# Performance work log

Hardware: AMD Instinct MI355X
Metric: run time of the kernel (lower is better)

## Reference

```python
import jax, jax.numpy as jnp
import numpy as np
from jax.scipy.linalg import expm

D = 12   # Fock cutoff dimension
M = 4    # qumodes per circuit
L = 2    # CVNN layers
K = M * (M - 1) // 2  # beamsplitters per interferometer
B = 1024

def _lad():
    # annihilation operator a in truncated Fock basis
    return jnp.diag(jnp.sqrt(jnp.arange(1, D, dtype=jnp.float32)), k=1).astype(jnp.complex64)

def _disp_gen(rr, ph):
    # generator of Displacement(r, phi): alpha*adag - conj(alpha)*a
    lad = _lad()
    alpha = (rr * jnp.exp(1j * ph)).astype(jnp.complex64)
    return alpha * lad.conj().T - jnp.conj(alpha) * lad

def _squeeze_mat(rr, ph):
    lad = _lad()
    z = (rr * jnp.exp(1j * ph)).astype(jnp.complex64)
    a2 = lad @ lad
    return expm(0.5 * (jnp.conj(z) * a2 - z * a2.conj().T))

def _rot_diag(ph):
    n = jnp.arange(D, dtype=jnp.float32)
    return jnp.exp(1j * ph * n).astype(jnp.complex64)

def _kerr_diag(kap):
    n = jnp.arange(D, dtype=jnp.float32)
    return jnp.exp(1j * kap * n * n).astype(jnp.complex64)

def _bs_mat(th, ph):
    # Beamsplitter exp(theta*(e^{i phi} a b^dag - e^{-i phi} a^dag b)) on D^2 space
    lad = _lad()
    eye = jnp.eye(D, dtype=jnp.complex64)
    a1 = jnp.kron(lad, eye)
    a2 = jnp.kron(eye, lad)
    H = th * (jnp.exp(1j * ph) * (a1 @ a2.conj().T) - jnp.exp(-1j * ph) * (a1.conj().T @ a2))
    return expm(H.astype(jnp.complex64)).reshape(D, D, D, D)

def _apply_1mode(psi, U, mode):
    psi = jnp.moveaxis(psi, mode + 1, -1)
    psi = psi @ U.T
    return jnp.moveaxis(psi, -1, mode + 1)

def _apply_1mode_batched(psi, U, mode):
    psi = jnp.moveaxis(psi, mode + 1, -1)
    psi = jnp.einsum('bij,b...j->b...i', U, psi)
    return jnp.moveaxis(psi, -1, mode + 1)

def _apply_diag(psi, d, mode):
    shape = [1] * psi.ndim
    shape[mode + 1] = D
    return psi * d.reshape(shape)

def _apply_2mode(psi, G, mode):
    psi = jnp.moveaxis(psi, (mode + 1, mode + 2), (-2, -1))
    psi = jnp.einsum('ijkl,...kl->...ij', G, psi)
    return jnp.moveaxis(psi, (-2, -1), (mode + 1, mode + 2))

def _interferometer(psi, theta, phi, varphi):
    # PennyLane rectangular (Clements) mesh, then per-mode rotations
    n = 0
    for ll in range(M):
        for kk in range(M - 1):
            if (ll + kk) % 2 != 1:
                psi = _apply_2mode(psi, _bs_mat(theta[n], phi[n]), kk)
                n += 1
    for m in range(M):
        psi = _apply_diag(psi, _rot_diag(varphi[m]), m)
    return psi

def _forward(x, theta_1, phi_1, varphi_1, r, phi_r, theta_2, phi_2, varphi_2, a, phi_a, k):
    b = x.shape[0]
    psi = jnp.zeros((b,) + (D,) * M, dtype=jnp.complex64)
    psi = psi.at[(slice(None),) + (0,) * M].set(1.0)  # vacuum
    # Amplitude_Phase encoding: Displacement(x[:, m], x[:, m+M]) on mode m
    for m in range(M):
        U = jax.vmap(lambda rr, ph: expm(_disp_gen(rr, ph)))(x[:, m], x[:, m + M])
        psi = _apply_1mode_batched(psi, U, m)
    # CVNeuralNetLayers
    for l in range(L):
        psi = _interferometer(psi, theta_1[l], phi_1[l], varphi_1[l])
        for m in range(M):
            psi = _apply_1mode(psi, _squeeze_mat(r[l, m], phi_r[l, m]), m)
        psi = _interferometer(psi, theta_2[l], phi_2[l], varphi_2[l])
        for m in range(M):
            psi = _apply_1mode(psi, expm(_disp_gen(a[l, m], phi_a[l, m])), m)
            psi = _apply_diag(psi, _kerr_diag(k[l, m]), m)
    # X-quadrature expvals (SF convention hbar=2: X = a + adag)
    lad = _lad()
    Xmat = lad + lad.conj().T
    sum_axes = tuple(range(1, M + 1))
    outs = [jnp.real(jnp.sum(jnp.conj(psi) * _apply_1mode(psi, Xmat, m), axis=sum_axes)) for m in range(M)]
    return jnp.stack(outs, axis=1)

def setup_inputs():
    key = jax.random.key(0)
    ks = jax.random.split(key, 12)
    tp = 2.0 * np.pi
    return {
        'x': jax.random.normal(ks[0], (B, 2 * M), dtype=jnp.float32),
        'theta_1': tp * jax.random.uniform(ks[1], (L, K), dtype=jnp.float32),
        'phi_1': tp * jax.random.uniform(ks[2], (L, K), dtype=jnp.float32),
        'varphi_1': tp * jax.random.uniform(ks[3], (L, M), dtype=jnp.float32),
        'r': 0.1 * jax.random.uniform(ks[4], (L, M), dtype=jnp.float32),
        'phi_r': tp * jax.random.uniform(ks[5], (L, M), dtype=jnp.float32),
        'theta_2': tp * jax.random.uniform(ks[6], (L, K), dtype=jnp.float32),
        'phi_2': tp * jax.random.uniform(ks[7], (L, K), dtype=jnp.float32),
        'varphi_2': tp * jax.random.uniform(ks[8], (L, M), dtype=jnp.float32),
        'a': 0.1 * jax.random.uniform(ks[9], (L, M), dtype=jnp.float32),
        'phi_a': tp * jax.random.uniform(ks[10], (L, M), dtype=jnp.float32),
        'k': tp * jax.random.uniform(ks[11], (L, M), dtype=jnp.float32),
    }

def reference(x, theta_1, phi_1, varphi_1, r, phi_r, theta_2, phi_2, varphi_2, a, phi_a, k):
    return _forward(x, theta_1, phi_1, varphi_1, r, phi_r, theta_2, phi_2, varphi_2, a, phi_a, k)
```

## Files before the change

### kernel.cpp

```cpp
#include <hip/hip_runtime.h>
#include <math.h>

#define D4 20736
#define ST 14
#define SST 168
#define KP 18

typedef float c32 __attribute__((ext_vector_type(2)));

__device__ __forceinline__ c32 C2(float x, float y) { c32 r; r.x = x; r.y = y; return r; }
#define CZERO C2(0.f, 0.f)

__device__ __forceinline__ c32 cmul(c32 a, c32 b) {
  return C2(a.x * b.x - a.y * b.y, a.x * b.y + a.y * b.x);
}
__device__ __forceinline__ c32 cfma_s(c32 a, c32 b, c32 acc) {
  acc.x = fmaf(a.x, b.x, fmaf(-a.y, b.y, acc.x));
  acc.y = fmaf(a.x, b.y, fmaf(a.y, b.x, acc.y));
  return acc;
}
__device__ __forceinline__ c32 cfma(c32 g, c32 v, c32 acc) {
  c32 t, d;
  asm("v_pk_fma_f32 %0, %1, %2, %3 op_sel_hi:[0,1,1]"
      : "=v"(t) : "v"(g), "v"(v), "v"(acc));
  asm("v_pk_fma_f32 %0, %1, %2, %3 op_sel:[1,1,0] op_sel_hi:[1,0,1] neg_lo:[1,0,0]"
      : "=v"(d) : "v"(g), "v"(v), "v"(t));
  return d;
}
__device__ __forceinline__ c32 get2(const float4* w, int n) {
  float4 q = w[n >> 1];
  return (n & 1) ? C2(q.z, q.w) : C2(q.x, q.y);
}
__device__ __forceinline__ float4 pack2(c32 a, c32 b) {
  return make_float4(a.x, a.y, b.x, b.y);
}

__constant__ int d_secoff[24] = {0,1,5,14,30,55,91,140,204,285,385,506,650,
                                 771,871,952,1016,1065,1101,1126,1142,1151,1155,1156};

__constant__ unsigned char d_perm[144] = {
  11,22,33,44,55,66,77,88,99,110,121,132,
  10,21,32,43,54,65,76,87,98,109,120,
  23,34,45,56,67,78,89,100,111,122,133,
  9,20,31,42,53,64,75,86,97,108,
  35,46,57,68,79,90,101,112,123,134,
  8,19,30,41,52,63,74,85,96,
  47,58,69,80,91,102,113,124,135,
  7,18,29,40,51,62,73,84,
  59,70,81,92,103,114,125,136,
  6,17,28,39,50,61,72,
  71,82,93,104,115,126,137,
  5,16,27,38,49,60,
  83,94,105,116,127,138,
  4,15,26,37,48,
  95,106,117,128,139,
  3,14,25,36,
  107,118,129,140,
  2,13,24,
  119,130,141,
  1,12,
  131,142,
  0,
  143
};

struct RM { int goff, sz, a0, da, r0, dr; };
__device__ __forceinline__ RM rmeta(int r) {
  const int i = r / 12, j = r - 12 * i, N = i + j;
  const bool up = (N <= 11);
  RM m;
  m.sz = (up ? N : 22 - N) + 1;
  const int lo = up ? 0 : (N - 11);
  m.goff = d_secoff[N] + (i - lo);
  m.a0 = up ? N : (143 + N);
  m.da = up ? 13 : -13;
  m.r0 = up ? N : (121 + N);
  m.dr = up ? 11 : -11;
  return m;
}

__device__ void small_expm(c32* A, c32* S, c32* P, c32* T, float* red, int sz, int tid) {
  const int n2 = sz * sz;
  if (tid < sz) {
    float s = 0.f;
    for (int j = 0; j < sz; ++j) { c32 v = A[tid * sz + j]; s += sqrtf(fmaf(v.x, v.x, v.y * v.y)); }
    red[tid] = s;
  }
  __syncthreads();
  float nrm = 0.f;
  for (int i = 0; i < sz; ++i) nrm = fmaxf(nrm, red[i]);
  int sp = 0;
  while (nrm > 0.35f && sp < 24) { nrm *= 0.5f; ++sp; }
  const float scale = ldexpf(1.f, -sp);
  for (int e = tid; e < n2; e += 64) { A[e].x *= scale; A[e].y *= scale; }
  __syncthreads();
  for (int e = tid; e < n2; e += 64) {
    c32 a = A[e];
    P[e] = a;
    if ((e / sz) == (e % sz)) a.x += 1.f;
    S[e] = a;
  }
  __syncthreads();
  for (int k = 2; k <= 12; ++k) {
    const float inv = 1.f / (float)k;
    for (int e = tid; e < n2; e += 64) {
      int i = e / sz, j = e - i * sz;
      c32 acc = CZERO;
      for (int q = 0; q < sz; ++q) acc = cfma_s(P[i * sz + q], A[q * sz + j], acc);
      acc.x *= inv; acc.y *= inv;
      T[e] = acc;
    }
    __syncthreads();
    for (int e = tid; e < n2; e += 64) {
      c32 t = T[e];
      P[e] = t;
      S[e].x += t.x; S[e].y += t.y;
    }
    __syncthreads();
  }
  for (int q = 0; q < sp; ++q) {
    for (int e = tid; e < n2; e += 64) {
      int i = e / sz, j = e - i * sz;
      c32 acc = CZERO;
      for (int w = 0; w < sz; ++w) acc = cfma_s(S[i * sz + w], S[w * sz + j], acc);
      T[e] = acc;
    }
    __syncthreads();
    for (int e = tid; e < n2; e += 64) S[e] = T[e];
    __syncthreads();
  }
}

__global__ __launch_bounds__(64) void prep_disp(const float* __restrict__ x, c32* __restrict__ c0) {
  __shared__ c32 A[144], S[144], P[144], T[144];
  __shared__ float red[12];
  const int tid = threadIdx.x;
  const int b = blockIdx.x >> 2, m = blockIdx.x & 3;
  const float rr = x[b * 8 + m], ph = x[b * 8 + 4 + m];
  float sn, cs;
  sincosf(ph, &sn, &cs);
  const c32 alpha = C2(rr * cs, rr * sn);
  for (int e = tid; e < 144; e += 64) A[e] = CZERO;
  __syncthreads();
  if (tid < 11) {
    float sq = sqrtf((float)(tid + 1));
    A[(tid + 1) * 12 + tid] = C2(alpha.x * sq, alpha.y * sq);
    A[tid * 12 + tid + 1] = C2(-alpha.x * sq, alpha.y * sq);
  }
  __syncthreads();
  small_expm(A, S, P, T, red, 12, tid);
  if (tid < 12) c0[(size_t)blockIdx.x * 12 + tid] = S[tid * 12];
}

__global__ __launch_bounds__(64) void prep_bs(const float* __restrict__ th1, const float* __restrict__ ph1,
                                              const float* __restrict__ th2, const float* __restrict__ ph2,
                                              c32* __restrict__ BS) {
  __shared__ c32 A[144], S[144], P[144], T[144];
  __shared__ float red[12];
  const int tid = threadIdx.x;
  const int g = blockIdx.x / 23, N = blockIdx.x % 23;
  const int l = g / 12, rem = g % 12, w = rem / 6, gi = rem % 6;
  const float th = (w ? th2 : th1)[l * 6 + gi];
  const float ph = (w ? ph2 : ph1)[l * 6 + gi];
  const int lo = (N > 11) ? (N - 11) : 0;
  const int sz = (N <= 11) ? (N + 1) : (23 - N);
  float sn, cs;
  sincosf(ph, &sn, &cs);
  for (int e = tid; e < sz * sz; e += 64) A[e] = CZERO;
  __syncthreads();
  if (tid + 1 < sz) {
    int t = tid + 1;
    float s1 = th * sqrtf((float)((lo + t) * (N - lo - t + 1)));
    A[(t - 1) * sz + t] = C2(cs * s1, sn * s1);
    A[t * sz + t - 1] = C2(-cs * s1, sn * s1);
  }
  __syncthreads();
  small_expm(A, S, P, T, red, sz, tid);
  c32* dst = BS + (size_t)g * 1156 + d_secoff[N];
  const bool upSec = (N <= 11);
  for (int e = tid; e < sz * sz; e += 64) {
    int p = e / sz, q = e - p * sz;
    int qs = upSec ? q : (sz - 1 - q);
    dst[q * sz + p] = S[p * sz + qs];
  }
}

__global__ __launch_bounds__(64) void prep_p(const float* __restrict__ r_, const float* __restrict__ phir,
                                             const float* __restrict__ vphi1,
                                             const float* __restrict__ a_, const float* __restrict__ phia,
                                             const float* __restrict__ vphi2, const float* __restrict__ kk,
                                             c32* __restrict__ P1, c32* __restrict__ P2) {
  __shared__ c32 A[144], S[144], P[144], T[144];
  __shared__ float red[12];
  const int tid = threadIdx.x;
  const int which = blockIdx.x >> 3, lm = blockIdx.x & 7;
  for (int e = tid; e < 144; e += 64) A[e] = CZERO;
  __syncthreads();
  if (which == 0) {
    const float rv = r_[lm], pv = phir[lm];
    float sn, cs;
    sincosf(pv, &sn, &cs);
    const c32 z = C2(rv * cs, rv * sn);
    if (tid < 10) {
      float sq = 0.5f * sqrtf((float)((tid + 1) * (tid + 2)));
      A[tid * 12 + tid + 2] = C2(z.x * sq, -z.y * sq);
      A[(tid + 2) * 12 + tid] = C2(-z.x * sq, -z.y * sq);
    }
  } else {
    const float av = a_[lm], pv = phia[lm];
    float sn, cs;
    sincosf(pv, &sn, &cs);
    const c32 alpha = C2(av * cs, av * sn);
    if (tid < 11) {
      float sq = sqrtf((float)(tid + 1));
      A[(tid + 1) * 12 + tid] = C2(alpha.x * sq, alpha.y * sq);
      A[tid * 12 + tid + 1] = C2(-alpha.x * sq, alpha.y * sq);
    }
  }
  __syncthreads();
  small_expm(A, S, P, T, red, 12, tid);
  if (which == 0) {
    const float vp = vphi1[lm];
    for (int e = tid; e < 144; e += 64) {
      int j = e % 12;
      float sn, cs;
      sincosf(vp * (float)j, &sn, &cs);
      P1[(size_t)lm * 144 + e] = cmul(S[e], C2(cs, sn));
    }
  } else {
    const float vp = vphi2[lm], kv = kk[lm];
    for (int e = tid; e < 144; e += 64) {
      int i = e / 12, j = e % 12;
      float sn1, cs1, sn2, cs2;
      sincosf(vp * (float)j, &sn1, &cs1);
      float ang = kv * (float)i;
      ang *= (float)i;
      sincosf(ang, &sn2, &cs2);
      P2[(size_t)lm * 144 + e] = cmul(C2(cs2, sn2), cmul(S[e], C2(cs1, sn1)));
    }
  }
}

__global__ __launch_bounds__(256, 6) void k123_kernel(
    c32* __restrict__ psi,
    const c32* __restrict__ gbs23, const c32* __restrict__ gbs12,
    const c32* __restrict__ gu1, const c32* __restrict__ gu2, const c32* __restrict__ gu3) {
  __shared__ __align__(16) c32 buf[2016];
  __shared__ c32 gate[1168];
  const int tid = threadIdx.x;
  c32 pf[5];
#pragma unroll
  for (int k = 0; k < 5; ++k) {
    int e = tid + 256 * k;
    pf[k] = (e < 1156) ? gbs12[e] : CZERO;
  }
  c32 pf3 = (gu3 && tid < 144) ? gu3[tid] : CZERO;
  if (gu1) for (int e = tid; e < 144; e += 256) buf[ST * e + 12] = gu1[e];
  if (gu2) for (int e = tid; e < 144; e += 256) buf[ST * e + 13] = gu2[e];
  for (int e = tid; e < 1156; e += 256) gate[e] = gbs23[e];
  c32* slab = psi + (size_t)blockIdx.x * 1728;
  for (int v = tid; v < 864; v += 256) {
    float4 q = ((const float4*)slab)[v];
    *((float4*)buf + 7 * (v / 6) + (v % 6)) = q;
  }
  __syncthreads();
  const int rb = (tid < 144) ? (int)d_perm[tid] : 0;
  RM m;
  if (tid < 144) m = rmeta(rb);
  c32 acc[12];
  if (tid < 144) {
#pragma unroll
    for (int n = 0; n < 12; ++n) acc[n] = CZERO;
    int a = m.a0, go = m.goff;
    for (int t = 0; t < m.sz; ++t) {
      c32 g = gate[go];
      go += m.sz;
#pragma unroll
      for (int n = 0; n < 12; ++n) acc[n] = cfma(g, buf[SST * n + a], acc[n]);
      a += m.da;
    }
  }
  __syncthreads();
  if (tid < 144) {
    const int wr = ST * (rb / 12) + (rb % 12);
#pragma unroll
    for (int n = 0; n < 12; ++n) buf[SST * n + wr] = acc[n];
  }
#pragma unroll
  for (int k = 0; k < 5; ++k) {
    int e = tid + 256 * k;
    if (e < 1156) gate[e] = pf[k];
  }
  __syncthreads();
  if (tid < 144) {
#pragma unroll
    for (int n = 0; n < 12; ++n) acc[n] = CZERO;
    int rho = m.r0, go = m.goff;
    for (int t = 0; t < m.sz; ++t) {
      c32 g = gate[go];
      go += m.sz;
      const float4* ip = (const float4*)buf + 7 * rho;
      float4 w[6];
#pragma unroll
      for (int q = 0; q < 6; ++q) w[q] = ip[q];
#pragma unroll
      for (int n = 0; n < 12; ++n) acc[n] = cfma(g, get2(w, n), acc[n]);
      rho += m.dr;
    }
  }
  __syncthreads();
  if (tid < 144) {
    float4* op = (float4*)buf + 7 * rb;
#pragma unroll
    for (int q = 0; q < 6; ++q) op[q] = pack2(acc[2 * q], acc[2 * q + 1]);
  }
  if (gu3 && tid < 144) gate[tid] = pf3;
  if (gu1) {
    __syncthreads();
    if (tid < 144) {
      const int p = tid >> 1, h = tid & 1;
      const int k2 = p / 12, n2 = p - 12 * (p / 12);
      c32 a0[6], a1[6];
#pragma unroll
      for (int n = 0; n < 6; ++n) { a0[n] = CZERO; a1[n] = CZERO; }
#pragma unroll
      for (int j = 0; j < 12; ++j) {
        c32 g0 = buf[ST * ((2 * k2) * 12 + j) + 12];
        c32 g1 = buf[ST * ((2 * k2 + 1) * 12 + j) + 12];
        const float4* ip = (const float4*)buf + 7 * (12 * j + n2) + 3 * h;
        float4 w0 = ip[0], w1 = ip[1], w2 = ip[2];
        c32 v[6] = {C2(w0.x,w0.y), C2(w0.z,w0.w), C2(w1.x,w1.y),
                    C2(w1.z,w1.w), C2(w2.x,w2.y), C2(w2.z,w2.w)};
#pragma unroll
        for (int n = 0; n < 6; ++n) {
          a0[n] = cfma(g0, v[n], a0[n]);
          a1[n] = cfma(g1, v[n], a1[n]);
        }
      }
#pragma unroll
      for (int n = 0; n < 6; ++n) { acc[n] = a0[n]; acc[6 + n] = a1[n]; }
    }
    __syncthreads();
    if (tid < 144) {
      const int p = tid >> 1, h = tid & 1;
      const int k2 = p / 12, n2 = p - 12 * (p / 12);
      float4* opA = (float4*)buf + 7 * ((2 * k2) * 12 + n2) + 3 * h;
      float4* opB = (float4*)buf + 7 * ((2 * k2 + 1) * 12 + n2) + 3 * h;
      opA[0] = pack2(acc[0], acc[1]); opA[1] = pack2(acc[2], acc[3]); opA[2] = pack2(acc[4], acc[5]);
      opB[0] = pack2(acc[6], acc[7]); opB[1] = pack2(acc[8], acc[9]); opB[2] = pack2(acc[10], acc[11]);
    }
  }
  if (gu2) {
    __syncthreads();
    if (tid < 144) {
      const int p = tid >> 1, h = tid & 1;
      const int n1 = p / 6, k2 = p - 6 * (p / 6);
      c32 a0[6], a1[6];
#pragma unroll
      for (int n = 0; n < 6; ++n) { a0[n] = CZERO; a1[n] = CZERO; }
#pragma unroll
      for (int j = 0; j < 12; ++j) {
        c32 g0 = buf[ST * ((2 * k2) * 12 + j) + 13];
        c32 g1 = buf[ST * ((2 * k2 + 1) * 12 + j) + 13];
        const float4* ip = (const float4*)buf + 7 * (12 * n1 + j) + 3 * h;
        float4 w0 = ip[0], w1 = ip[1], w2 = ip[2];
        c32 v[6] = {C2(w0.x,w0.y), C2(w0.z,w0.w), C2(w1.x,w1.y),
                    C2(w1.z,w1.w), C2(w2.x,w2.y), C2(w2.z,w2.w)};
#pragma unroll
        for (int n = 0; n < 6; ++n) {
          a0[n] = cfma(g0, v[n], a0[n]);
          a1[n] = cfma(g1, v[n], a1[n]);
        }
      }
#pragma unroll
      for (int n = 0; n < 6; ++n) { acc[n] = a0[n]; acc[6 + n] = a1[n]; }
    }
    __syncthreads();
    if (tid < 144) {
      const int p = tid >> 1, h = tid & 1;
      const int n1 = p / 6, k2 = p - 6 * (p / 6);
      float4* opA = (float4*)buf + 7 * (12 * n1 + 2 * k2) + 3 * h;
      float4* opB = (float4*)buf + 7 * (12 * n1 + 2 * k2 + 1) + 3 * h;
      opA[0] = pack2(acc[0], acc[1]); opA[1] = pack2(acc[2], acc[3]); opA[2] = pack2(acc[4], acc[5]);
      opB[0] = pack2(acc[6], acc[7]); opB[1] = pack2(acc[8], acc[9]); opB[2] = pack2(acc[10], acc[11]);
    }
  }
  if (gu3) {
    __syncthreads();
    if (tid < 144) {
      const float4* ip = (const float4*)buf + 7 * tid;
      float4 wv[6];
#pragma unroll
      for (int q = 0; q < 6; ++q) wv[q] = ip[q];
      float4* op = (float4*)buf + 7 * tid;
#pragma unroll
      for (int cpair = 0; cpair < 6; ++cpair) {
        c32 s0 = CZERO, s1 = CZERO;
#pragma unroll
        for (int j = 0; j < 12; ++j) {
          c32 v = get2(wv, j);
          s0 = cfma(gate[(2 * cpair) * 12 + j], v, s0);
          s1 = cfma(gate[(2 * cpair + 1) * 12 + j], v, s1);
        }
        op[cpair] = pack2(s0, s1);
      }
    }
  }
  __syncthreads();
  for (int v = tid; v < 864; v += 256) {
    ((float4*)slab)[v] = *((const float4*)buf + 7 * (v / 6) + (v % 6));
  }
}

__global__ __launch_bounds__(256, 5) void k01_kernel(
    c32* __restrict__ psi, const c32* __restrict__ c0,
    const c32* __restrict__ gu0, const c32* __restrict__ gbs) {
  __shared__ __align__(16) c32 buf[2592];
  __shared__ c32 gate[1168];
  __shared__ c32 cv[4][12];
  const int tid = threadIdx.x;
  const int b = blockIdx.x / 9, t = blockIdx.x % 9;
  if (gu0) for (int e = tid; e < 144; e += 256) buf[KP * e + 16] = gu0[e];
  if (gbs) for (int e = tid; e < 1156; e += 256) gate[e] = gbs[e];
  c32* gbase = psi + (size_t)b * D4 + t * 16;
  if (c0) {
    if (tid < 48) cv[tid / 12][tid % 12] = c0[(size_t)b * 48 + tid];
    __syncthreads();
    for (int e = tid; e < 2304; e += 256) {
      int row = e >> 4, q = e & 15;
      int cc = 16 * t + q, n2 = cc / 12, n3 = cc - 12 * n2;
      buf[KP * row + q] =
          cmul(cmul(cv[0][row / 12], cv[1][row % 12]), cmul(cv[2][n2], cv[3][n3]));
    }
  } else {
    for (int e = tid; e < 1152; e += 256) {
      int row = e >> 3, q = e & 7;
      ((float4*)(buf + row * KP))[q] = ((const float4*)(gbase + (size_t)row * 144))[q];
    }
  }
  __syncthreads();
  c32 acc[16];
  if (gu0) {
    if (tid < 144) {
      const int p = tid >> 1, h = tid & 1;
      const int k2 = p / 12, n1 = p - 12 * (p / 12);
      c32 a0[8], a1[8];
#pragma unroll
      for (int n = 0; n < 8; ++n) { a0[n] = CZERO; a1[n] = CZERO; }
#pragma unroll
      for (int j = 0; j < 12; ++j) {
        c32 g0 = buf[((2 * k2) * 12 + j) * KP + 16];
        c32 g1 = buf[((2 * k2 + 1) * 12 + j) * KP + 16];
        const float4* ip = (const float4*)(buf + (12 * j + n1) * KP) + 4 * h;
        float4 w[4];
#pragma unroll
        for (int q = 0; q < 4; ++q) w[q] = ip[q];
#pragma unroll
        for (int n = 0; n < 8; ++n) {
          c32 v = get2(w, n);
          a0[n] = cfma(g0, v, a0[n]);
          a1[n] = cfma(g1, v, a1[n]);
        }
      }
#pragma unroll
      for (int n = 0; n < 8; ++n) { acc[n] = a0[n]; acc[8 + n] = a1[n]; }
    }
    __syncthreads();
    if (tid < 144) {
      const int p = tid >> 1, h = tid & 1;
      const int k2 = p / 12, n1 = p - 12 * (p / 12);
      float4* opA = (float4*)(buf + ((2 * k2) * 12 + n1) * KP) + 4 * h;
      float4* opB = (float4*)(buf + ((2 * k2 + 1) * 12 + n1) * KP) + 4 * h;
#pragma unroll
      for (int q = 0; q < 4; ++q) {
        opA[q] = pack2(acc[2 * q], acc[2 * q + 1]);
        opB[q] = pack2(acc[8 + 2 * q], acc[8 + 2 * q + 1]);
      }
    }
    __syncthreads();
  }
  if (gbs) {
    const int rb = (tid < 144) ? (int)d_perm[tid] : 0;
    if (tid < 144) {
      const RM m = rmeta(rb);
#pragma unroll
      for (int n = 0; n < 16; ++n) acc[n] = CZERO;
      int rho = m.r0, go = m.goff;
      for (int tk = 0; tk < m.sz; ++tk) {
        c32 g = gate[go];
        go += m.sz;
        const float4* ip = (const float4*)(buf + rho * KP);
        float4 w[8];
#pragma unroll
        for (int q = 0; q < 8; ++q) w[q] = ip[q];
#pragma unroll
        for (int n = 0; n < 16; ++n) acc[n] = cfma(g, get2(w, n), acc[n]);
        rho += m.dr;
      }
    }
    __syncthreads();
    if (tid < 144) {
      float4* op = (float4*)(buf + rb * KP);
#pragma unroll
      for (int q = 0; q < 8; ++q) op[q] = pack2(acc[2 * q], acc[2 * q + 1]);
    }
    __syncthreads();
  }
  for (int e = tid; e < 1152; e += 256) {
    int row = e >> 3, q = e & 7;
    ((float4*)(gbase + (size_t)row * 144))[q] = ((const float4*)(buf + row * KP))[q];
  }
}

__global__ __launch_bounds__(256) void expval_kernel(const c32* __restrict__ psi, float* __restrict__ out) {
  __shared__ float red[1024];
  __shared__ float sq2[12];
  const int tid = threadIdx.x, b = blockIdx.x;
  if (tid < 12) sq2[tid] = 2.f * sqrtf((float)(tid + 1));
  __syncthreads();
  const c32* base = psi + (size_t)b * D4;
  float a0 = 0.f, a1 = 0.f, a2 = 0.f, a3 = 0.f;
  for (int e = tid; e < D4; e += 256) {
    c32 p = base[e];
    int n3 = e % 12, t = e / 12;
    int n2 = t % 12; t /= 12;
    int n1 = t % 12, n0 = t / 12;
    if (n3 < 11) { c32 q = base[e + 1];    a3 = fmaf(sq2[n3], fmaf(p.x, q.x, p.y * q.y), a3); }
    if (n2 < 11) { c32 q = base[e + 12];   a2 = fmaf(sq2[n2], fmaf(p.x, q.x, p.y * q.y), a2); }
    if (n1 < 11) { c32 q = base[e + 144];  a1 = fmaf(sq2[n1], fmaf(p.x, q.x, p.y * q.y), a1); }
    if (n0 < 11) { c32 q = base[e + 1728]; a0 = fmaf(sq2[n0], fmaf(p.x, q.x, p.y * q.y), a0); }
  }
  red[tid * 4 + 0] = a0; red[tid * 4 + 1] = a1; red[tid * 4 + 2] = a2; red[tid * 4 + 3] = a3;
  __syncthreads();
  for (int s = 128; s > 0; s >>= 1) {
    if (tid < s) {
      red[tid * 4 + 0] += red[(tid + s) * 4 + 0];
      red[tid * 4 + 1] += red[(tid + s) * 4 + 1];
      red[tid * 4 + 2] += red[(tid + s) * 4 + 2];
      red[tid * 4 + 3] += red[(tid + s) * 4 + 3];
    }
    __syncthreads();
  }
  if (tid < 4) out[b * 4 + tid] = red[tid];
}

extern "C" void kernel_launch(void* const* d_in, const int* in_sizes, int n_in,
                              void* d_out, int out_size, void* d_ws, size_t ws_size,
                              hipStream_t stream) {
  const float* x      = (const float*)d_in[0];
  const float* theta1 = (const float*)d_in[1];
  const float* phi1   = (const float*)d_in[2];
  const float* vphi1  = (const float*)d_in[3];
  const float* r_     = (const float*)d_in[4];
  const float* phir   = (const float*)d_in[5];
  const float* theta2 = (const float*)d_in[6];
  const float* phi2   = (const float*)d_in[7];
  const float* vphi2  = (const float*)d_in[8];
  const float* a_     = (const float*)d_in[9];
  const float* phia   = (const float*)d_in[10];
  const float* kk     = (const float*)d_in[11];
  float* out = (float*)d_out;

  const size_t PSI_OFF = 0;
  const size_t C0_OFF  = 169869312;
  const size_t P1_OFF  = C0_OFF + 393216;
  const size_t P2_OFF  = P1_OFF + 9216;
  const size_t BS_OFF  = P2_OFF + 9216;
  const size_t NEED    = BS_OFF + 221952;
  if (ws_size < NEED) return;

  char* ws = (char*)d_ws;
  c32* psi = (c32*)(ws + PSI_OFF);
  c32* c0  = (c32*)(ws + C0_OFF);
  c32* P1  = (c32*)(ws + P1_OFF);
  c32* P2  = (c32*)(ws + P2_OFF);
  c32* BS  = (c32*)(ws + BS_OFF);

  prep_disp<<<dim3(4096), dim3(64), 0, stream>>>(x, c0);
  prep_bs<<<dim3(552), dim3(64), 0, stream>>>(theta1, phi1, theta2, phi2, BS);
  prep_p<<<dim3(16), dim3(64), 0, stream>>>(r_, phir, vphi1, a_, phia, vphi2, kk, P1, P2);

  for (int l = 0; l < 2; ++l) {
    c32* bsl = BS + (size_t)l * 12 * 1156;
    const c32* c0arg = (l == 0) ? c0 : (const c32*)nullptr;
    const c32* u0pre = (l == 0) ? (const c32*)nullptr : (const c32*)(P2 + (size_t)(l - 1) * 4 * 144);
    k01_kernel<<<dim3(9216), dim3(256), 0, stream>>>(psi, c0arg, u0pre, bsl + 0 * 1156);
    k123_kernel<<<dim3(12288), dim3(256), 0, stream>>>(psi, bsl + 1 * 1156, bsl + 2 * 1156,
                                                       nullptr, nullptr, nullptr);
    k01_kernel<<<dim3(9216), dim3(256), 0, stream>>>(psi, nullptr, nullptr, bsl + 3 * 1156);
    k123_kernel<<<dim3(12288), dim3(256), 0, stream>>>(psi, bsl + 4 * 1156, bsl + 5 * 1156,
                                                       P1 + (size_t)(l * 4 + 1) * 144,
                                                       P1 + (size_t)(l * 4 + 2) * 144,
                                                       P1 + (size_t)(l * 4 + 3) * 144);
    k01_kernel<<<dim3(9216), dim3(256), 0, stream>>>(psi, nullptr, P1 + (size_t)(l * 4 + 0) * 144, bsl + 6 * 1156);
    k123_kernel<<<dim3(12288), dim3(256), 0, stream>>>(psi, bsl + 7 * 1156, bsl + 8 * 1156,
                                                       nullptr, nullptr, nullptr);
    k01_kernel<<<dim3(9216), dim3(256), 0, stream>>>(psi, nullptr, nullptr, bsl + 9 * 1156);
    k123_kernel<<<dim3(12288), dim3(256), 0, stream>>>(psi, bsl + 10 * 1156, bsl + 11 * 1156,
                                                       P2 + (size_t)(l * 4 + 1) * 144,
                                                       P2 + (size_t)(l * 4 + 2) * 144,
                                                       P2 + (size_t)(l * 4 + 3) * 144);
  }
  k01_kernel<<<dim3(9216), dim3(256), 0, stream>>>(psi, nullptr, P2 + (size_t)(1 * 4 + 0) * 144, nullptr);
  expval_kernel<<<dim3(1024), dim3(256), 0, stream>>>(psi, out);
}
```

Measured before the change: 1.966 ms.

## Pair beamsplitter output rows per thread and split columns across thread pairs

Reorganises the photon-number-sector beamsplitter contractions so each thread computes two adjacent output rows of a sector over half the columns, sharing each loaded input vector across two gate coefficients. A new packed pair table replaces the per-row permutation, and 156 threads now take part where 144 did before. The single-mode gate matrices are stored transposed in shared memory, which changes their read addressing. This aims to cut shared-memory loads per FMA and per-thread register pressure, at the cost of some wasted work on odd-sized sectors, where the second row's gate is zeroed.

```diff
diff --git a/kernel.cpp b/kernel.cpp
--- a/kernel.cpp
+++ b/kernel.cpp
@@ -38,44 +38,49 @@
 __constant__ int d_secoff[24] = {0,1,5,14,30,55,91,140,204,285,385,506,650,
                                  771,871,952,1016,1065,1101,1126,1142,1151,1155,1156};
 
-__constant__ unsigned char d_perm[144] = {
-  11,22,33,44,55,66,77,88,99,110,121,132,
-  10,21,32,43,54,65,76,87,98,109,120,
-  23,34,45,56,67,78,89,100,111,122,133,
-  9,20,31,42,53,64,75,86,97,108,
-  35,46,57,68,79,90,101,112,123,134,
-  8,19,30,41,52,63,74,85,96,
-  47,58,69,80,91,102,113,124,135,
-  7,18,29,40,51,62,73,84,
-  59,70,81,92,103,114,125,136,
-  6,17,28,39,50,61,72,
-  71,82,93,104,115,126,137,
-  5,16,27,38,49,60,
-  83,94,105,116,127,138,
-  4,15,26,37,48,
-  95,106,117,128,139,
-  3,14,25,36,
-  107,118,129,140,
-  2,13,24,
-  119,130,141,
-  1,12,
-  131,142,
+__constant__ unsigned char d_pp[78] = {
+  88,89,90,91,92,93,
+  80,81,82,83,84,85,
+  96,97,98,99,100,101,
+  72,73,74,75,76,
+  104,105,106,107,108,
+  64,65,66,67,68,
+  112,113,114,115,116,
+  56,57,58,59,
+  120,121,122,123,
+  48,49,50,51,
+  128,129,130,131,
+  40,41,42,
+  136,137,138,
+  32,33,34,
+  144,145,146,
+  24,25,
+  152,153,
+  16,17,
+  160,161,
+  8,
+  168,
   0,
-  143
+  176
 };
 
-struct RM { int goff, sz, a0, da, r0, dr; };
-__device__ __forceinline__ RM rmeta(int r) {
-  const int i = r / 12, j = r - 12 * i, N = i + j;
+struct PM { int sz, goff, a0, da, r0, dr, w1, w2; bool v1; };
+__device__ __forceinline__ PM pmeta(int pr) {
+  const int code = d_pp[pr];
+  const int N = code >> 3, k = code & 7;
   const bool up = (N <= 11);
-  RM m;
+  PM m;
   m.sz = (up ? N : 22 - N) + 1;
   const int lo = up ? 0 : (N - 11);
-  m.goff = d_secoff[N] + (i - lo);
+  const int i0 = lo + 2 * k;
+  m.v1 = (2 * k + 1 < m.sz);
+  m.goff = d_secoff[N] + 2 * k;
   m.a0 = up ? N : (143 + N);
   m.da = up ? 13 : -13;
   m.r0 = up ? N : (121 + N);
   m.dr = up ? 11 : -11;
+  m.w1 = 13 * i0 + N;
+  m.w2 = 11 * i0 + N;
   return m;
 }
 
@@ -255,8 +260,8 @@
     pf[k] = (e < 1156) ? gbs12[e] : CZERO;
   }
   c32 pf3 = (gu3 && tid < 144) ? gu3[tid] : CZERO;
-  if (gu1) for (int e = tid; e < 144; e += 256) buf[ST * e + 12] = gu1[e];
-  if (gu2) for (int e = tid; e < 144; e += 256) buf[ST * e + 13] = gu2[e];
+  if (gu1) for (int e = tid; e < 144; e += 256) buf[ST * ((e % 12) * 12 + e / 12) + 12] = gu1[e];
+  if (gu2) for (int e = tid; e < 144; e += 256) buf[ST * ((e % 12) * 12 + e / 12) + 13] = gu2[e];
   for (int e = tid; e < 1156; e += 256) gate[e] = gbs23[e];
   c32* slab = psi + (size_t)blockIdx.x * 1728;
   for (int v = tid; v < 864; v += 256) {
@@ -264,27 +269,37 @@
     *((float4*)buf + 7 * (v / 6) + (v % 6)) = q;
   }
   __syncthreads();
-  const int rb = (tid < 144) ? (int)d_perm[tid] : 0;
-  RM m;
-  if (tid < 144) m = rmeta(rb);
-  c32 acc[12];
-  if (tid < 144) {
-#pragma unroll
-    for (int n = 0; n < 12; ++n) acc[n] = CZERO;
-    int a = m.a0, go = m.goff;
+  const int pr = tid >> 1, h = tid & 1;
+  PM m;
+  if (tid < 156) m = pmeta(pr);
+  c32 acc0[6], acc1[6];
+  if (tid < 156) {
+#pragma unroll
+    for (int n = 0; n < 6; ++n) { acc0[n] = CZERO; acc1[n] = CZERO; }
+    int a = m.a0 + 1008 * h, go = m.goff;
     for (int t = 0; t < m.sz; ++t) {
-      c32 g = gate[go];
+      c32 g0 = gate[go];
+      c32 g1 = gate[go + 1];
+      if (!m.v1) g1 = CZERO;
       go += m.sz;
 #pragma unroll
-      for (int n = 0; n < 12; ++n) acc[n] = cfma(g, buf[SST * n + a], acc[n]);
+      for (int n = 0; n < 6; ++n) {
+        c32 v = buf[SST * n + a];
+        acc0[n] = cfma(g0, v, acc0[n]);
+        acc1[n] = cfma(g1, v, acc1[n]);
+      }
       a += m.da;
     }
   }
   __syncthreads();
-  if (tid < 144) {
-    const int wr = ST * (rb / 12) + (rb % 12);
-#pragma unroll
-    for (int n = 0; n < 12; ++n) buf[SST * n + wr] = acc[n];
+  if (tid < 156) {
+    const int w0 = m.w1 + 1008 * h;
+#pragma unroll
+    for (int n = 0; n < 6; ++n) buf[SST * n + w0] = acc0[n];
+    if (m.v1) {
+#pragma unroll
+      for (int n = 0; n < 6; ++n) buf[SST * n + w0 + 13] = acc1[n];
+    }
   }
 #pragma unroll
   for (int k = 0; k < 5; ++k) {
@@ -292,97 +307,103 @@
     if (e < 1156) gate[e] = pf[k];
   }
   __syncthreads();
-  if (tid < 144) {
-#pragma unroll
-    for (int n = 0; n < 12; ++n) acc[n] = CZERO;
+  if (tid < 156) {
+#pragma unroll
+    for (int n = 0; n < 6; ++n) { acc0[n] = CZERO; acc1[n] = CZERO; }
     int rho = m.r0, go = m.goff;
     for (int t = 0; t < m.sz; ++t) {
-      c32 g = gate[go];
+      c32 g0 = gate[go];
+      c32 g1 = gate[go + 1];
+      if (!m.v1) g1 = CZERO;
       go += m.sz;
-      const float4* ip = (const float4*)buf + 7 * rho;
-      float4 w[6];
-#pragma unroll
-      for (int q = 0; q < 6; ++q) w[q] = ip[q];
-#pragma unroll
-      for (int n = 0; n < 12; ++n) acc[n] = cfma(g, get2(w, n), acc[n]);
+      const float4* ip = (const float4*)buf + 7 * rho + 3 * h;
+      float4 w0 = ip[0], w1 = ip[1], w2 = ip[2];
+      c32 v[6] = {C2(w0.x,w0.y), C2(w0.z,w0.w), C2(w1.x,w1.y),
+                  C2(w1.z,w1.w), C2(w2.x,w2.y), C2(w2.z,w2.w)};
+#pragma unroll
+      for (int n = 0; n < 6; ++n) {
+        acc0[n] = cfma(g0, v[n], acc0[n]);
+        acc1[n] = cfma(g1, v[n], acc1[n]);
+      }
       rho += m.dr;
     }
   }
   __syncthreads();
-  if (tid < 144) {
-    float4* op = (float4*)buf + 7 * rb;
-#pragma unroll
-    for (int q = 0; q < 6; ++q) op[q] = pack2(acc[2 * q], acc[2 * q + 1]);
+  if (tid < 156) {
+    float4* opA = (float4*)buf + 7 * m.w2 + 3 * h;
+    opA[0] = pack2(acc0[0], acc0[1]);
+    opA[1] = pack2(acc0[2], acc0[3]);
+    opA[2] = pack2(acc0[4], acc0[5]);
+    if (m.v1) {
+      float4* opB = (float4*)buf + 7 * (m.w2 + 11) + 3 * h;
+      opB[0] = pack2(acc1[0], acc1[1]);
+      opB[1] = pack2(acc1[2], acc1[3]);
+      opB[2] = pack2(acc1[4], acc1[5]);
+    }
   }
   if (gu3 && tid < 144) gate[tid] = pf3;
   if (gu1) {
     __syncthreads();
     if (tid < 144) {
-      const int p = tid >> 1, h = tid & 1;
+      const int p = tid >> 1, hh = tid & 1;
       const int k2 = p / 12, n2 = p - 12 * (p / 12);
-      c32 a0[6], a1[6];
-#pragma unroll
-      for (int n = 0; n < 6; ++n) { a0[n] = CZERO; a1[n] = CZERO; }
+#pragma unroll
+      for (int n = 0; n < 6; ++n) { acc0[n] = CZERO; acc1[n] = CZERO; }
 #pragma unroll
       for (int j = 0; j < 12; ++j) {
-        c32 g0 = buf[ST * ((2 * k2) * 12 + j) + 12];
-        c32 g1 = buf[ST * ((2 * k2 + 1) * 12 + j) + 12];
-        const float4* ip = (const float4*)buf + 7 * (12 * j + n2) + 3 * h;
+        c32 g0 = buf[ST * (j * 12 + 2 * k2) + 12];
+        c32 g1 = buf[ST * (j * 12 + 2 * k2 + 1) + 12];
+        const float4* ip = (const float4*)buf + 7 * (12 * j + n2) + 3 * hh;
         float4 w0 = ip[0], w1 = ip[1], w2 = ip[2];
         c32 v[6] = {C2(w0.x,w0.y), C2(w0.z,w0.w), C2(w1.x,w1.y),
                     C2(w1.z,w1.w), C2(w2.x,w2.y), C2(w2.z,w2.w)};
 #pragma unroll
         for (int n = 0; n < 6; ++n) {
-          a0[n] = cfma(g0, v[n], a0[n]);
-          a1[n] = cfma(g1, v[n], a1[n]);
+          acc0[n] = cfma(g0, v[n], acc0[n]);
+          acc1[n] = cfma(g1, v[n], acc1[n]);
         }
       }
-#pragma unroll
-      for (int n = 0; n < 6; ++n) { acc[n] = a0[n]; acc[6 + n] = a1[n]; }
     }
     __syncthreads();
     if (tid < 144) {
-      const int p = tid >> 1, h = tid & 1;
+      const int p = tid >> 1, hh = tid & 1;
       const int k2 = p / 12, n2 = p - 12 * (p / 12);
-      float4* opA = (float4*)buf + 7 * ((2 * k2) * 12 + n2) + 3 * h;
-      float4* opB = (float4*)buf + 7 * ((2 * k2 + 1) * 12 + n2) + 3 * h;
-      opA[0] = pack2(acc[0], acc[1]); opA[1] = pack2(acc[2], acc[3]); opA[2] = pack2(acc[4], acc[5]);
-      opB[0] = pack2(acc[6], acc[7]); opB[1] = pack2(acc[8], acc[9]); opB[2] = pack2(acc[10], acc[11]);
+      float4* opA = (float4*)buf + 7 * ((2 * k2) * 12 + n2) + 3 * hh;
+      float4* opB = (float4*)buf + 7 * ((2 * k2 + 1) * 12 + n2) + 3 * hh;
+      opA[0] = pack2(acc0[0], acc0[1]); opA[1] = pack2(acc0[2], acc0[3]); opA[2] = pack2(acc0[4], acc0[5]);
+      opB[0] = pack2(acc1[0], acc1[1]); opB[1] = pack2(acc1[2], acc1[3]); opB[2] = pack2(acc1[4], acc1[5]);
     }
   }
   if (gu2) {
     __syncthreads();
     if (tid < 144) {
-      const int p = tid >> 1, h = tid & 1;
+      const int p = tid >> 1, hh = tid & 1;
       const int n1 = p / 6, k2 = p - 6 * (p / 6);
-      c32 a0[6], a1[6];
-#pragma unroll
-      for (int n = 0; n < 6; ++n) { a0[n] = CZERO; a1[n] = CZERO; }
+#pragma unroll
+      for (int n = 0; n < 6; ++n) { acc0[n] = CZERO; acc1[n] = CZERO; }
 #pragma unroll
       for (int j = 0; j < 12; ++j) {
-        c32 g0 = buf[ST * ((2 * k2) * 12 + j) + 13];
-        c32 g1 = buf[ST * ((2 * k2 + 1) * 12 + j) + 13];
-        const float4* ip = (const float4*)buf + 7 * (12 * n1 + j) + 3 * h;
+        c32 g0 = buf[ST * (j * 12 + 2 * k2) + 13];
+        c32 g1 = buf[ST * (j * 12 + 2 * k2 + 1) + 13];
+        const float4* ip = (const float4*)buf + 7 * (12 * n1 + j) + 3 * hh;
         float4 w0 = ip[0], w1 = ip[1], w2 = ip[2];
         c32 v[6] = {C2(w0.x,w0.y), C2(w0.z,w0.w), C2(w1.x,w1.y),
                     C2(w1.z,w1.w), C2(w2.x,w2.y), C2(w2.z,w2.w)};
 #pragma unroll
         for (int n = 0; n < 6; ++n) {
-          a0[n] = cfma(g0, v[n], a0[n]);
-          a1[n] = cfma(g1, v[n], a1[n]);
+          acc0[n] = cfma(g0, v[n], acc0[n]);
+          acc1[n] = cfma(g1, v[n], acc1[n]);
         }
       }
-#pragma unroll
-      for (int n = 0; n < 6; ++n) { acc[n] = a0[n]; acc[6 + n] = a1[n]; }
     }
     __syncthreads();
     if (tid < 144) {
-      const int p = tid >> 1, h = tid & 1;
+      const int p = tid >> 1, hh = tid & 1;
       const int n1 = p / 6, k2 = p - 6 * (p / 6);
-      float4* opA = (float4*)buf + 7 * (12 * n1 + 2 * k2) + 3 * h;
-      float4* opB = (float4*)buf + 7 * (12 * n1 + 2 * k2 + 1) + 3 * h;
-      opA[0] = pack2(acc[0], acc[1]); opA[1] = pack2(acc[2], acc[3]); opA[2] = pack2(acc[4], acc[5]);
-      opB[0] = pack2(acc[6], acc[7]); opB[1] = pack2(acc[8], acc[9]); opB[2] = pack2(acc[10], acc[11]);
+      float4* opA = (float4*)buf + 7 * (12 * n1 + 2 * k2) + 3 * hh;
+      float4* opB = (float4*)buf + 7 * (12 * n1 + 2 * k2 + 1) + 3 * hh;
+      opA[0] = pack2(acc0[0], acc0[1]); opA[1] = pack2(acc0[2], acc0[3]); opA[2] = pack2(acc0[4], acc0[5]);
+      opB[0] = pack2(acc1[0], acc1[1]); opB[1] = pack2(acc1[2], acc1[3]); opB[2] = pack2(acc1[4], acc1[5]);
     }
   }
   if (gu3) {
@@ -420,7 +441,7 @@
   __shared__ c32 cv[4][12];
   const int tid = threadIdx.x;
   const int b = blockIdx.x / 9, t = blockIdx.x % 9;
-  if (gu0) for (int e = tid; e < 144; e += 256) buf[KP * e + 16] = gu0[e];
+  if (gu0) for (int e = tid; e < 144; e += 256) buf[KP * ((e % 12) * 12 + e / 12) + 16] = gu0[e];
   if (gbs) for (int e = tid; e < 1156; e += 256) gate[e] = gbs[e];
   c32* gbase = psi + (size_t)b * D4 + t * 16;
   if (c0) {
@@ -439,70 +460,79 @@
     }
   }
   __syncthreads();
-  c32 acc[16];
+  c32 acc0[8], acc1[8];
   if (gu0) {
     if (tid < 144) {
-      const int p = tid >> 1, h = tid & 1;
+      const int p = tid >> 1, hh = tid & 1;
       const int k2 = p / 12, n1 = p - 12 * (p / 12);
-      c32 a0[8], a1[8];
-#pragma unroll
-      for (int n = 0; n < 8; ++n) { a0[n] = CZERO; a1[n] = CZERO; }
+#pragma unroll
+      for (int n = 0; n < 8; ++n) { acc0[n] = CZERO; acc1[n] = CZERO; }
 #pragma unroll
       for (int j = 0; j < 12; ++j) {
-        c32 g0 = buf[((2 * k2) * 12 + j) * KP + 16];
-        c32 g1 = buf[((2 * k2 + 1) * 12 + j) * KP + 16];
-        const float4* ip = (const float4*)(buf + (12 * j + n1) * KP) + 4 * h;
+        c32 g0 = buf[KP * (j * 12 + 2 * k2) + 16];
+        c32 g1 = buf[KP * (j * 12 + 2 * k2 + 1) + 16];
+        const float4* ip = (const float4*)(buf + (12 * j + n1) * KP) + 4 * hh;
         float4 w[4];
 #pragma unroll
         for (int q = 0; q < 4; ++q) w[q] = ip[q];
 #pragma unroll
         for (int n = 0; n < 8; ++n) {
           c32 v = get2(w, n);
-          a0[n] = cfma(g0, v, a0[n]);
-          a1[n] = cfma(g1, v, a1[n]);
+          acc0[n] = cfma(g0, v, acc0[n]);
+          acc1[n] = cfma(g1, v, acc1[n]);
         }
       }
-#pragma unroll
-      for (int n = 0; n < 8; ++n) { acc[n] = a0[n]; acc[8 + n] = a1[n]; }
     }
     __syncthreads();
     if (tid < 144) {
-      const int p = tid >> 1, h = tid & 1;
+      const int p = tid >> 1, hh = tid & 1;
       const int k2 = p / 12, n1 = p - 12 * (p / 12);
-      float4* opA = (float4*)(buf + ((2 * k2) * 12 + n1) * KP) + 4 * h;
-      float4* opB = (float4*)(buf + ((2 * k2 + 1) * 12 + n1) * KP) + 4 * h;
+      float4* opA = (float4*)(buf + ((2 * k2) * 12 + n1) * KP) + 4 * hh;
+      float4* opB = (float4*)(buf + ((2 * k2 + 1) * 12 + n1) * KP) + 4 * hh;
 #pragma unroll
       for (int q = 0; q < 4; ++q) {
-        opA[q] = pack2(acc[2 * q], acc[2 * q + 1]);
-        opB[q] = pack2(acc[8 + 2 * q], acc[8 + 2 * q + 1]);
+        opA[q] = pack2(acc0[2 * q], acc0[2 * q + 1]);
+        opB[q] = pack2(acc1[2 * q], acc1[2 * q + 1]);
       }
     }
     __syncthreads();
   }
   if (gbs) {
-    const int rb = (tid < 144) ? (int)d_perm[tid] : 0;
-    if (tid < 144) {
-      const RM m = rmeta(rb);
-#pragma unroll
-      for (int n = 0; n < 16; ++n) acc[n] = CZERO;
+    const int pr = tid >> 1, h = tid & 1;
+    PM m;
+    if (tid < 156) {
+      m = pmeta(pr);
+#pragma unroll
+      for (int n = 0; n < 8; ++n) { acc0[n] = CZERO; acc1[n] = CZERO; }
       int rho = m.r0, go = m.goff;
       for (int tk = 0; tk < m.sz; ++tk) {
-        c32 g = gate[go];
+        c32 g0 = gate[go];
+        c32 g1 = gate[go + 1];
+        if (!m.v1) g1 = CZERO;
         go += m.sz;
-        const float4* ip = (const float4*)(buf + rho * KP);
-        float4 w[8];
-#pragma unroll
-        for (int q = 0; q < 8; ++q) w[q] = ip[q];
-#pragma unroll
-        for (int n = 0; n < 16; ++n) acc[n] = cfma(g, get2(w, n), acc[n]);
+        const float4* ip = (const float4*)(buf + rho * KP) + 4 * h;
+        float4 w[4];
+#pragma unroll
+        for (int q = 0; q < 4; ++q) w[q] = ip[q];
+#pragma unroll
+        for (int n = 0; n < 8; ++n) {
+          c32 v = get2(w, n);
+          acc0[n] = cfma(g0, v, acc0[n]);
+          acc1[n] = cfma(g1, v, acc1[n]);
+        }
         rho += m.dr;
       }
     }
     __syncthreads();
-    if (tid < 144) {
-      float4* op = (float4*)(buf + rb * KP);
-#pragma unroll
-      for (int q = 0; q < 8; ++q) op[q] = pack2(acc[2 * q], acc[2 * q + 1]);
+    if (tid < 156) {
+      float4* opA = (float4*)(buf + m.w2 * KP) + 4 * h;
+#pragma unroll
+      for (int q = 0; q < 4; ++q) opA[q] = pack2(acc0[2 * q], acc0[2 * q + 1]);
+      if (m.v1) {
+        float4* opB = (float4*)(buf + (m.w2 + 11) * KP) + 4 * h;
+#pragma unroll
+        for (int q = 0; q < 4; ++q) opB[q] = pack2(acc1[2 * q], acc1[2 * q + 1]);
+      }
     }
     __syncthreads();
   }
```

After: 1.888 ms. -4.0%, faster.
